# Kernel tuning notes

Measured on AMD Instinct MI355X. Metric: run time of the kernel, lower is better.

Reference implementation:

```python
import jax, jax.numpy as jnp
import numpy as np


def setup_inputs() -> dict:
    key = jax.random.key(0)
    k1, k2 = jax.random.split(key)
    B, T, D, E = 4, 4096, 2048, 64
    x = jax.random.normal(k1, (B, T, D), dtype=jnp.float32)
    # nn.Linear default init ~ U(-1/sqrt(D), 1/sqrt(D)); scaled normal is fine for a numeric baseline
    W = jax.random.normal(k2, (D, E), dtype=jnp.float32) * (1.0 / np.sqrt(D))
    b = jnp.zeros((E,), dtype=jnp.float32)
    return {"x": x, "W": W, "b": b}


TOPK = 2


def reference(x, W, b):
    # logits: (B, T, E)
    logits = jnp.einsum("btd,de->bte", x, W) + b
    probs = jax.nn.softmax(logits, axis=-1)
    topk_vals, topk_idx = jax.lax.top_k(probs, TOPK)
    return topk_idx, topk_vals
```

## Files before the change

### kernel.cpp

```cpp
#include <hip/hip_runtime.h>
#include <math.h>


#define D_DIM 2048
#define E_DIM 64
#define M_DIM 16384
#define RM 16
#define BKC 64
#define NCH 32
#define XSTR 68

typedef _Float16 half8 __attribute__((ext_vector_type(8)));
typedef float floatx4 __attribute__((ext_vector_type(4)));
typedef unsigned int uint;

__global__ __launch_bounds__(256) void split_w_kernel(
    const float* __restrict__ Wm, _Float16* __restrict__ wsT)
{
    const int tid = threadIdx.x;
    const int n   = tid & 63;
    const int kk0 = tid >> 6;
    const int g   = blockIdx.x;
    #pragma unroll
    for (int r = 0; r < 8; r++) {
        const int kk = kk0 + r * 4;
        const float v = Wm[(size_t)(g * 32 + kk) * E_DIM + n];
        const _Float16 h = (_Float16)v;
        const _Float16 l = (_Float16)((v - (float)h) * 2048.0f);
        const int t = n >> 4, cc = n & 15, qd = kk >> 3, j = kk & 7;
        const size_t base = (size_t)((g * 4 + t) * 2) * 512 + (size_t)(qd * 16 + cc) * 8 + j;
        wsT[base]       = h;
        wsT[base + 512] = l;
    }
}

__global__ __launch_bounds__(256, 4) void router_mfma_kernel(
    const float* __restrict__ x, const _Float16* __restrict__ wsT,
    const float* __restrict__ bias, float* __restrict__ out)
{
    __shared__ uint xbuf[2][RM * XSTR];

    const int tid  = threadIdx.x;
    const int lane = tid & 63;
    const int wave = tid >> 6;
    const int c    = lane & 15;
    const int quad = lane >> 4;
    const int rs   = tid >> 4;
    const int c4   = tid & 15;
    const int r0   = blockIdx.x * RM;

    const float*    xg = x   + (size_t)(r0 + rs) * D_DIM + c4 * 4;
    const _Float16* wt = wsT + (size_t)wave * 1024 + (size_t)lane * 8;

    floatx4 accm = {0.f, 0.f, 0.f, 0.f};
    floatx4 accl = {0.f, 0.f, 0.f, 0.f};
    float4 ra, rb;

    auto xload = [&](int n) -> float4 {
        const int nn = n < NCH ? n : NCH - 1;
        return *reinterpret_cast<const float4*>(xg + nn * BKC);
    };
    auto stage = [&](int buf, const float4& v4) {
        const float v[4] = {v4.x, v4.y, v4.z, v4.w};
        uint p[4];
        #pragma unroll
        for (int q = 0; q < 4; q++) {
            const _Float16 h = (_Float16)v[q];
            const _Float16 l = (_Float16)((v[q] - (float)h) * 2048.0f);
            p[q] = (uint)__builtin_bit_cast(unsigned short, h)
                 | ((uint)__builtin_bit_cast(unsigned short, l) << 16);
        }
        *reinterpret_cast<uint4*>(&xbuf[buf][rs * XSTR + c4 * 4]) =
            make_uint4(p[0], p[1], p[2], p[3]);
    };
    auto compute = [&](int buf, int n) {
        #pragma unroll
        for (int s = 0; s < 2; s++) {
            const _Float16* wp = wt + (size_t)(2 * n + s) * 4096;
            const half8 wh = *reinterpret_cast<const half8*>(wp);
            const half8 wl = *reinterpret_cast<const half8*>(wp + 512);
            const uint* rp = &xbuf[buf][c * XSTR + s * 32 + quad * 8];
            uint u8[8];
            *reinterpret_cast<uint4*>(u8)     = *reinterpret_cast<const uint4*>(rp);
            *reinterpret_cast<uint4*>(u8 + 4) = *reinterpret_cast<const uint4*>(rp + 4);
            uint hh[4], ll[4];
            #pragma unroll
            for (int q = 0; q < 4; q++) {
                hh[q] = (u8[2 * q] & 0xffffu) | (u8[2 * q + 1] << 16);
                ll[q] = (u8[2 * q] >> 16) | (u8[2 * q + 1] & 0xffff0000u);
            }
            const half8 ah = __builtin_bit_cast(half8, make_uint4(hh[0], hh[1], hh[2], hh[3]));
            const half8 al = __builtin_bit_cast(half8, make_uint4(ll[0], ll[1], ll[2], ll[3]));
            accm = __builtin_amdgcn_mfma_f32_16x16x32_f16(ah, wh, accm, 0, 0, 0);
            accl = __builtin_amdgcn_mfma_f32_16x16x32_f16(al, wh, accl, 0, 0, 0);
            accl = __builtin_amdgcn_mfma_f32_16x16x32_f16(ah, wl, accl, 0, 0, 0);
        }
    };
    auto barrier_lds = [&]() {
        asm volatile("s_waitcnt lgkmcnt(0)" ::: "memory");
        __builtin_amdgcn_s_barrier();
        asm volatile("" ::: "memory");
    };

    ra = xload(0);
    rb = xload(1);
    stage(0, ra);
    ra = xload(2);

    #pragma unroll 1
    for (int n = 0; n < NCH; n += 2) {
        barrier_lds();
        compute(0, n);
        stage(1, rb);
        rb = xload(n + 3);
        barrier_lds();
        compute(1, n + 1);
        if (n + 2 < NCH) stage(0, ra);
        ra = xload(n + 4);
    }

    __syncthreads();
    float* red = reinterpret_cast<float*>(&xbuf[0][0]);
    const float scale = 1.0f / 2048.0f;
    #pragma unroll
    for (int i = 0; i < 4; i++)
        red[(quad * 4 + i) * 65 + wave * 16 + c] = accm[i] + accl[i] * scale;
    __syncthreads();

    if (wave != 0) return;

    float bvt[4];
    #pragma unroll
    for (int t = 0; t < 4; t++) bvt[t] = bias[c + 16 * t];

    #pragma unroll
    for (int i = 0; i < 4; i++) {
        const int row = quad * 4 + i;
        float lt[4];
        #pragma unroll
        for (int t = 0; t < 4; t++)
            lt[t] = red[row * 65 + 16 * t + c] + bvt[t];
        const float l0 = lt[0], l1 = lt[1], l2 = lt[2], l3 = lt[3];

        float m = fmaxf(fmaxf(l0, l1), fmaxf(l2, l3));
        #pragma unroll
        for (int off = 1; off < 16; off <<= 1)
            m = fmaxf(m, __shfl_xor(m, off, 64));

        const float e0 = expf(l0 - m), e1 = expf(l1 - m);
        const float e2 = expf(l2 - m), e3 = expf(l3 - m);
        float s = e0 + e1 + e2 + e3;
        #pragma unroll
        for (int off = 1; off < 16; off <<= 1)
            s += __shfl_xor(s, off, 64);

        const float p0 = e0 / s, p1 = e1 / s, p2 = e2 / s, p3 = e3 / s;

        const unsigned long long ka =
            ((unsigned long long)__float_as_uint(p0) << 32) | (unsigned long long)(63 - c);
        const unsigned long long kb_ =
            ((unsigned long long)__float_as_uint(p1) << 32) | (unsigned long long)(47 - c);
        const unsigned long long kc_ =
            ((unsigned long long)__float_as_uint(p2) << 32) | (unsigned long long)(31 - c);
        const unsigned long long kd =
            ((unsigned long long)__float_as_uint(p3) << 32) | (unsigned long long)(15 - c);

        unsigned long long hi1 = ka > kb_ ? ka : kb_, lo1 = ka > kb_ ? kb_ : ka;
        unsigned long long hi2 = kc_ > kd ? kc_ : kd, lo2 = kc_ > kd ? kd : kc_;
        unsigned long long k1 = hi1 > hi2 ? hi1 : hi2;
        unsigned long long mn = hi1 > hi2 ? hi2 : hi1;
        unsigned long long mx = lo1 > lo2 ? lo1 : lo2;
        unsigned long long k2 = mn > mx ? mn : mx;

        #pragma unroll
        for (int off = 1; off < 16; off <<= 1) {
            const unsigned long long o1 = __shfl_xor(k1, off, 64);
            const unsigned long long o2 = __shfl_xor(k2, off, 64);
            const unsigned long long n1 = k1 > o1 ? k1 : o1;
            const unsigned long long w1 = k1 > o1 ? o1 : k1;
            const unsigned long long w2 = k2 > o2 ? k2 : o2;
            k1 = n1;
            k2 = w1 > w2 ? w1 : w2;
        }

        if (c == 0) {
            const int gr = r0 + row;
            out[gr * 2 + 0] = (float)(63 - (int)(k1 & 0xFFFFFFFFull));
            out[gr * 2 + 1] = (float)(63 - (int)(k2 & 0xFFFFFFFFull));
            out[M_DIM * 2 + gr * 2 + 0] = __uint_as_float((unsigned)(k1 >> 32));
            out[M_DIM * 2 + gr * 2 + 1] = __uint_as_float((unsigned)(k2 >> 32));
        }
    }
}

extern "C" void kernel_launch(void* const* d_in, const int* in_sizes, int n_in,
                              void* d_out, int out_size, void* d_ws, size_t ws_size,
                              hipStream_t stream) {
    const float* x  = (const float*)d_in[0];
    const float* Wm = (const float*)d_in[1];
    const float* b  = (const float*)d_in[2];
    float* out = (float*)d_out;
    _Float16* wsT = (_Float16*)d_ws;

    split_w_kernel<<<dim3(64), dim3(256), 0, stream>>>(Wm, wsT);
    router_mfma_kernel<<<dim3(M_DIM / RM), dim3(256), 0, stream>>>(x, wsT, b, out);
}
```

Baseline: 210.8 us.

## Double block rows to 32 with 512 threads and prefetch W fragments ahead

```diff
diff --git a/kernel.cpp b/kernel.cpp
--- a/kernel.cpp
+++ b/kernel.cpp
@@ -5,7 +5,7 @@
 #define D_DIM 2048
 #define E_DIM 64
 #define M_DIM 16384
-#define RM 16
+#define RM 32
 #define BKC 64
 #define NCH 32
 #define XSTR 68
@@ -34,7 +34,7 @@
     }
 }
 
-__global__ __launch_bounds__(256, 4) void router_mfma_kernel(
+__global__ __launch_bounds__(512, 4) void router_mfma_kernel(
     const float* __restrict__ x, const _Float16* __restrict__ wsT,
     const float* __restrict__ bias, float* __restrict__ out)
 {
@@ -43,6 +43,8 @@
     const int tid  = threadIdx.x;
     const int lane = tid & 63;
     const int wave = tid >> 6;
+    const int et   = wave & 3;
+    const int tau  = wave >> 2;
     const int c    = lane & 15;
     const int quad = lane >> 4;
     const int rs   = tid >> 4;
@@ -50,15 +52,22 @@
     const int r0   = blockIdx.x * RM;
 
     const float*    xg = x   + (size_t)(r0 + rs) * D_DIM + c4 * 4;
-    const _Float16* wt = wsT + (size_t)wave * 1024 + (size_t)lane * 8;
+    const _Float16* wt = wsT + (size_t)et * 1024 + (size_t)lane * 8;
 
     floatx4 accm = {0.f, 0.f, 0.f, 0.f};
     floatx4 accl = {0.f, 0.f, 0.f, 0.f};
-    float4 ra, rb;
 
     auto xload = [&](int n) -> float4 {
         const int nn = n < NCH ? n : NCH - 1;
         return *reinterpret_cast<const float4*>(xg + nn * BKC);
+    };
+    auto loadWc = [&](int m, half8* wv) {
+        const int mm = m < NCH ? m : NCH - 1;
+        const _Float16* p0 = wt + (size_t)(2 * mm) * 4096;
+        wv[0] = *reinterpret_cast<const half8*>(p0);
+        wv[1] = *reinterpret_cast<const half8*>(p0 + 512);
+        wv[2] = *reinterpret_cast<const half8*>(p0 + 4096);
+        wv[3] = *reinterpret_cast<const half8*>(p0 + 4096 + 512);
     };
     auto stage = [&](int buf, const float4& v4) {
         const float v[4] = {v4.x, v4.y, v4.z, v4.w};
@@ -73,13 +82,10 @@
         *reinterpret_cast<uint4*>(&xbuf[buf][rs * XSTR + c4 * 4]) =
             make_uint4(p[0], p[1], p[2], p[3]);
     };
-    auto compute = [&](int buf, int n) {
+    auto compute = [&](int buf, const half8* wv) {
         #pragma unroll
         for (int s = 0; s < 2; s++) {
-            const _Float16* wp = wt + (size_t)(2 * n + s) * 4096;
-            const half8 wh = *reinterpret_cast<const half8*>(wp);
-            const half8 wl = *reinterpret_cast<const half8*>(wp + 512);
-            const uint* rp = &xbuf[buf][c * XSTR + s * 32 + quad * 8];
+            const uint* rp = &xbuf[buf][(tau * 16 + c) * XSTR + s * 32 + quad * 8];
             uint u8[8];
             *reinterpret_cast<uint4*>(u8)     = *reinterpret_cast<const uint4*>(rp);
             *reinterpret_cast<uint4*>(u8 + 4) = *reinterpret_cast<const uint4*>(rp + 4);
@@ -91,9 +97,9 @@
             }
             const half8 ah = __builtin_bit_cast(half8, make_uint4(hh[0], hh[1], hh[2], hh[3]));
             const half8 al = __builtin_bit_cast(half8, make_uint4(ll[0], ll[1], ll[2], ll[3]));
-            accm = __builtin_amdgcn_mfma_f32_16x16x32_f16(ah, wh, accm, 0, 0, 0);
-            accl = __builtin_amdgcn_mfma_f32_16x16x32_f16(al, wh, accl, 0, 0, 0);
-            accl = __builtin_amdgcn_mfma_f32_16x16x32_f16(ah, wl, accl, 0, 0, 0);
+            accm = __builtin_amdgcn_mfma_f32_16x16x32_f16(ah, wv[2 * s],     accm, 0, 0, 0);
+            accl = __builtin_amdgcn_mfma_f32_16x16x32_f16(al, wv[2 * s],     accl, 0, 0, 0);
+            accl = __builtin_amdgcn_mfma_f32_16x16x32_f16(ah, wv[2 * s + 1], accl, 0, 0, 0);
         }
     };
     auto barrier_lds = [&]() {
@@ -102,21 +108,32 @@
         asm volatile("" ::: "memory");
     };
 
-    ra = xload(0);
-    rb = xload(1);
-    stage(0, ra);
-    ra = xload(2);
+    float4 q0, q1, q2, q3;
+    half8 WA[4], WB[4];
+
+    q0 = xload(0); q1 = xload(1); q2 = xload(2); q3 = xload(3);
+    loadWc(0, WA);
+    stage(0, q0);
+    q0 = xload(4);
 
     #pragma unroll 1
-    for (int n = 0; n < NCH; n += 2) {
-        barrier_lds();
-        compute(0, n);
-        stage(1, rb);
-        rb = xload(n + 3);
-        barrier_lds();
-        compute(1, n + 1);
-        if (n + 2 < NCH) stage(0, ra);
-        ra = xload(n + 4);
+    for (int n = 0; n < NCH; n += 4) {
+        loadWc(n + 1, WB);
+        barrier_lds();
+        compute(0, WA);
+        stage(1, q1);  q1 = xload(n + 5);
+        loadWc(n + 2, WA);
+        barrier_lds();
+        compute(1, WB);
+        stage(0, q2);  q2 = xload(n + 6);
+        loadWc(n + 3, WB);
+        barrier_lds();
+        compute(0, WA);
+        stage(1, q3);  q3 = xload(n + 7);
+        loadWc(n + 4, WA);
+        barrier_lds();
+        compute(1, WB);
+        if (n + 4 < NCH) { stage(0, q0); q0 = xload(n + 8); }
     }
 
     __syncthreads();
@@ -124,10 +141,10 @@
     const float scale = 1.0f / 2048.0f;
     #pragma unroll
     for (int i = 0; i < 4; i++)
-        red[(quad * 4 + i) * 65 + wave * 16 + c] = accm[i] + accl[i] * scale;
+        red[(tau * 16 + quad * 4 + i) * 65 + et * 16 + c] = accm[i] + accl[i] * scale;
     __syncthreads();
 
-    if (wave != 0) return;
+    if (wave >= 2) return;
 
     float bvt[4];
     #pragma unroll
@@ -135,7 +152,7 @@
 
     #pragma unroll
     for (int i = 0; i < 4; i++) {
-        const int row = quad * 4 + i;
+        const int row = wave * 16 + quad * 4 + i;
         float lt[4];
         #pragma unroll
         for (int t = 0; t < 4; t++)
@@ -203,5 +220,5 @@
     _Float16* wsT = (_Float16*)d_ws;
 
     split_w_kernel<<<dim3(64), dim3(256), 0, stream>>>(Wm, wsT);
-    router_mfma_kernel<<<dim3(M_DIM / RM), dim3(256), 0, stream>>>(x, wsT, b, out);
+    router_mfma_kernel<<<dim3(M_DIM / RM), dim3(512), 0, stream>>>(x, wsT, b, out);
 }
```

Measured after the change: 209.8 us. Within noise of the previous version (-0.5%).
